# Kernel tuning notes

Measured on AMD Instinct MI355X. Metric: run time of the kernel, lower is better.

## Reference

```python
import jax, jax.numpy as jnp
import numpy as np

CHUNK = 128  # intra-chunk causal block size for the chunked linear-attention scan


def setup_inputs() -> dict:
    key = jax.random.key(0)
    ks = jax.random.split(key, 7)
    B, H, N, D, F = 1, 24, 4096, 128, 256
    q = jax.random.normal(ks[0], (B, H, N, D), dtype=jnp.float32)
    k = jax.random.normal(ks[1], (B, H, N, D), dtype=jnp.float32)
    v = jax.random.normal(ks[2], (B, H, N, D), dtype=jnp.float32)
    # fan-in scaling so phi features / accumulated state stay numerically sane
    w1 = jax.random.normal(ks[3], (F, D), dtype=jnp.float32) * (D ** -0.5)
    b1 = jax.random.normal(ks[4], (F,), dtype=jnp.float32) * 0.02
    w2 = jax.random.normal(ks[5], (F, F), dtype=jnp.float32) * (F ** -0.5)
    b2 = jax.random.normal(ks[6], (F,), dtype=jnp.float32) * 0.02
    return {"q": q, "k": k, "v": v, "w1": w1, "b1": b1, "w2": w2, "b2": b2}


def _phi(x, w1, b1, w2, b2):
    # Linear(D->F) -> SiLU -> Linear(F->F)
    h = jax.nn.silu(jnp.einsum('bnd,fd->bnf', x, w1) + b1)
    return jnp.einsum('bnf,gf->bng', h, w2) + b2


def _causal_scan(qp, kp, vf):
    # out_t = q_t . (sum_{s<=t} k_s v_s^T) / (t+1), chunked parallel form.
    BH, N, F = qp.shape
    D = vf.shape[-1]
    C = CHUNK
    nC = N // C
    qc = qp.reshape(BH, nC, C, F).transpose(1, 0, 2, 3)  # [nC,BH,C,F]
    kc = kp.reshape(BH, nC, C, F).transpose(1, 0, 2, 3)
    vc = vf.reshape(BH, nC, C, D).transpose(1, 0, 2, 3)
    offsets = (jnp.arange(nC) * C).astype(qp.dtype)
    mask = jnp.tril(jnp.ones((C, C), dtype=qp.dtype))  # include diagonal
    pos = jnp.arange(1, C + 1, dtype=qp.dtype)

    def step(w, inp):
        qb, kb, vb, off = inp
        inter = jnp.einsum('bcf,bfd->bcd', qb, w)
        attn = jnp.einsum('bcf,bsf->bcs', qb, kb) * mask
        intra = jnp.einsum('bcs,bsd->bcd', attn, vb)
        counts = off + pos  # global (token_idx + 1)
        out = (inter + intra) / counts[None, :, None]
        w = w + jnp.einsum('bcf,bcd->bfd', kb, vb)
        return w, out

    w0 = jnp.zeros((BH, F, D), dtype=qp.dtype)
    _, outs = jax.lax.scan(step, w0, (qc, kc, vc, offsets))  # outs [nC,BH,C,D]
    return outs.transpose(1, 0, 2, 3).reshape(BH, N, D)


def reference(q, k, v, w1, b1, w2, b2):
    B, H, N, D = q.shape
    qf = q.reshape(B * H, N, D)
    kf = k.reshape(B * H, N, D)
    vf = v.reshape(B * H, N, D)
    qp = _phi(qf, w1, b1, w2, b2)
    kp = _phi(kf, w1, b1, w2, b2)
    out_fwd = _causal_scan(qp, kp, vf)
    out_rev = _causal_scan(qp[:, ::-1], kp[:, ::-1], vf[:, ::-1])[:, ::-1]
    return (out_fwd + out_rev).reshape(B, H, N, D)
```

## Files before the change

kernel.cpp:

```cpp
#include <hip/hip_runtime.h>


typedef __attribute__((ext_vector_type(8))) _Float16 f16x8;
typedef __attribute__((ext_vector_type(4))) _Float16 f16x4;
typedef __attribute__((ext_vector_type(4))) float f32x4;

#define MFMA16(a, b, c) __builtin_amdgcn_mfma_f32_16x16x32_f16((a), (b), (c), 0, 0, 0)

constexpr int BH   = 24;
constexpr int NSEQ = 4096;
constexpr int DD   = 128;
constexpr int FF   = 256;
constexpr int CHK  = 128;
constexpr int NC   = NSEQ / CHK;
constexpr int NROWS = BH * NSEQ;

__global__ void prep_kernel(const float* __restrict__ w1, const float* __restrict__ w2,
                            _Float16* __restrict__ w1h, _Float16* __restrict__ w2h) {
  int i = blockIdx.x * 256 + threadIdx.x;
  if (i < FF * DD) w1h[i] = (_Float16)w1[i];
  if (i < FF * FF) w2h[i] = (_Float16)w2[i];
}

__global__ void vt_kernel(const float* __restrict__ v, _Float16* __restrict__ vT) {
  __shared__ __align__(16) _Float16 lt[128][136];
  int blk = blockIdx.x;
  int c = blk & 31, bh = blk >> 5;
  const float* vc = v + ((size_t)bh * NSEQ + c * CHK) * DD;
  int tid = threadIdx.x;
#pragma unroll
  for (int it = 0; it < 16; ++it) {
    int flat = it * 1024 + tid * 4;
    int s = flat >> 7, d0 = flat & 127;
    float4 xv = *(const float4*)&vc[(size_t)s * DD + d0];
    lt[d0 + 0][s] = (_Float16)xv.x;
    lt[d0 + 1][s] = (_Float16)xv.y;
    lt[d0 + 2][s] = (_Float16)xv.z;
    lt[d0 + 3][s] = (_Float16)xv.w;
  }
  __syncthreads();
#pragma unroll
  for (int it = 0; it < 8; ++it) {
    int flat = it * 256 + tid;
    int d = flat >> 4, sg = flat & 15;
    *(f16x8*)&vT[((size_t)bh * DD + d) * NSEQ + c * CHK + sg * 8] =
        *(const f16x8*)&lt[d][sg * 8];
  }
}

__global__ __launch_bounds__(512, 2)
void phi_kernel(const float* __restrict__ q, const float* __restrict__ k,
                const float* __restrict__ b1, const float* __restrict__ b2,
                const _Float16* __restrict__ w1h, const _Float16* __restrict__ w2h,
                _Float16* __restrict__ qp, _Float16* __restrict__ kp,
                _Float16* __restrict__ kpT) {
  __shared__ __align__(16) char smem[137216];
  _Float16 (*xs)[136]  = (_Float16(*)[136])smem;
  _Float16 (*w1s)[136] = (_Float16(*)[136])(smem + 34816);
  _Float16 (*hs)[264]  = (_Float16(*)[264])smem;
  _Float16 (*w2s)[136] = (_Float16(*)[136])(smem + 67584);
  int blk = blockIdx.x;
  const float* src;
  _Float16* dst;
  bool isk;
  int rb;
  if (blk < NROWS / 128) { src = q; dst = qp; rb = blk * 128; isk = false; }
  else                   { src = k; dst = kp; rb = (blk - NROWS / 128) * 128; isk = true; }
  int tid = threadIdx.x;
  int lane = tid & 63, wv = tid >> 6, lr = lane & 15, lq = lane >> 4;

#pragma unroll
  for (int it = 0; it < 8; ++it) {
    int flat = it * 512 + tid;
    int f = flat >> 4, cg = flat & 15;
    *(f16x8*)&w1s[f][cg * 8] = *(const f16x8*)&w1h[f * DD + cg * 8];
  }
#pragma unroll
  for (int it = 0; it < 8; ++it) {
    int flat = it * 512 + tid;
    int r = flat >> 5, dg = flat & 31;
    float4 xv = *(const float4*)&src[(size_t)(rb + r) * DD + dg * 4];
    f16x4 hv = {(_Float16)xv.x, (_Float16)xv.y, (_Float16)xv.z, (_Float16)xv.w};
    *(f16x4*)&xs[r][dg * 4] = hv;
  }
  __syncthreads();

  int wm1 = wv & 1, wn1 = wv >> 1;
  f32x4 acc[4][4] = {};
#pragma unroll
  for (int ks = 0; ks < 4; ++ks) {
    f16x8 av[4];
#pragma unroll
    for (int im = 0; im < 4; ++im)
      av[im] = *(const f16x8*)&xs[wm1 * 64 + im * 16 + lr][ks * 32 + lq * 8];
#pragma unroll
    for (int fn = 0; fn < 4; ++fn) {
      f16x8 bv = *(const f16x8*)&w1s[wn1 * 64 + fn * 16 + lr][ks * 32 + lq * 8];
#pragma unroll
      for (int im = 0; im < 4; ++im) acc[im][fn] = MFMA16(av[im], bv, acc[im][fn]);
    }
  }
  __syncthreads();

#pragma unroll
  for (int it = 0; it < 8; ++it) {
    int flat = it * 512 + tid;
    int g = flat >> 4, cg = flat & 15;
    *(f16x8*)&w2s[g][cg * 8] = *(const f16x8*)&w2h[(size_t)g * FF + cg * 8];
  }
#pragma unroll
  for (int im = 0; im < 4; ++im)
#pragma unroll
    for (int fn = 0; fn < 4; ++fn) {
      int f = wn1 * 64 + fn * 16 + lr;
      float bb = b1[f];
      int r0 = wm1 * 64 + im * 16 + lq * 4;
#pragma unroll
      for (int r = 0; r < 4; ++r) {
        float xv = acc[im][fn][r] + bb;
        hs[r0 + r][f] = (_Float16)(xv / (1.0f + __expf(-xv)));
      }
    }
  __syncthreads();

  int wmg = wv & 1, wng = wv >> 1;
  f32x4 ac2[4][4] = {};
#pragma unroll
  for (int ks = 0; ks < 4; ++ks) {
    f16x8 av[4];
#pragma unroll
    for (int im = 0; im < 4; ++im)
      av[im] = *(const f16x8*)&hs[wmg * 64 + im * 16 + lr][ks * 32 + lq * 8];
#pragma unroll
    for (int fn = 0; fn < 4; ++fn) {
      f16x8 bv = *(const f16x8*)&w2s[wng * 64 + fn * 16 + lr][ks * 32 + lq * 8];
#pragma unroll
      for (int im = 0; im < 4; ++im) ac2[im][fn] = MFMA16(av[im], bv, ac2[im][fn]);
    }
  }
  __syncthreads();
#pragma unroll
  for (int it = 0; it < 8; ++it) {
    int flat = it * 512 + tid;
    int g = flat >> 4, cg = flat & 15;
    *(f16x8*)&w2s[g][cg * 8] = *(const f16x8*)&w2h[(size_t)g * FF + 128 + cg * 8];
  }
  __syncthreads();
#pragma unroll
  for (int ks = 0; ks < 4; ++ks) {
    f16x8 av[4];
#pragma unroll
    for (int im = 0; im < 4; ++im)
      av[im] = *(const f16x8*)&hs[wmg * 64 + im * 16 + lr][128 + ks * 32 + lq * 8];
#pragma unroll
    for (int fn = 0; fn < 4; ++fn) {
      f16x8 bv = *(const f16x8*)&w2s[wng * 64 + fn * 16 + lr][ks * 32 + lq * 8];
#pragma unroll
      for (int im = 0; im < 4; ++im) ac2[im][fn] = MFMA16(av[im], bv, ac2[im][fn]);
    }
  }

  int bh = rb >> 12, s0 = rb & 4095;
#pragma unroll
  for (int im = 0; im < 4; ++im)
#pragma unroll
    for (int fn = 0; fn < 4; ++fn) {
      int g = wng * 64 + fn * 16 + lr;
      float bb = b2[g];
      int r0 = wmg * 64 + im * 16 + lq * 4;
#pragma unroll
      for (int r = 0; r < 4; ++r) {
        _Float16 val = (_Float16)(ac2[im][fn][r] + bb);
        dst[(size_t)(rb + r0 + r) * FF + g] = val;
        if (isk) kpT[((size_t)bh * FF + g) * NSEQ + s0 + r0 + r] = val;
      }
    }
}

__global__ __launch_bounds__(512, 2)
void s_kernel(const _Float16* __restrict__ vT, const _Float16* __restrict__ kpT,
              _Float16* __restrict__ S) {
  __shared__ __align__(16) _Float16 vt[128][136];
  __shared__ __align__(16) _Float16 kt[256][136];
  int blk = blockIdx.x;
  int c = blk & 31, bh = blk >> 5;
  int tid = threadIdx.x;
#pragma unroll
  for (int it = 0; it < 4; ++it) {
    int flat = it * 512 + tid;
    int d = flat >> 4, sg = flat & 15;
    *(f16x8*)&vt[d][sg * 8] = *(const f16x8*)&vT[((size_t)bh * DD + d) * NSEQ + c * CHK + sg * 8];
  }
#pragma unroll
  for (int it = 0; it < 8; ++it) {
    int flat = it * 512 + tid;
    int f = flat >> 4, sg = flat & 15;
    *(f16x8*)&kt[f][sg * 8] = *(const f16x8*)&kpT[((size_t)bh * FF + f) * NSEQ + c * CHK + sg * 8];
  }
  __syncthreads();
  int lane = tid & 63, wv = tid >> 6, lr = lane & 15, lq = lane >> 4;
  int wmd = wv & 1, wnf = wv >> 1;
  f32x4 acc[4][4] = {};
#pragma unroll
  for (int ks = 0; ks < 4; ++ks) {
    f16x8 av[4];
#pragma unroll
    for (int im = 0; im < 4; ++im)
      av[im] = *(const f16x8*)&vt[wmd * 64 + im * 16 + lr][ks * 32 + lq * 8];
#pragma unroll
    for (int fn = 0; fn < 4; ++fn) {
      f16x8 bv = *(const f16x8*)&kt[wnf * 64 + fn * 16 + lr][ks * 32 + lq * 8];
#pragma unroll
      for (int im = 0; im < 4; ++im) acc[im][fn] = MFMA16(av[im], bv, acc[im][fn]);
    }
  }
  _Float16* Sp = S + ((size_t)bh * NC + c) * (size_t)(DD * FF);
#pragma unroll
  for (int im = 0; im < 4; ++im)
#pragma unroll
    for (int fn = 0; fn < 4; ++fn) {
      int f = wnf * 64 + fn * 16 + lr;
#pragma unroll
      for (int r = 0; r < 4; ++r) {
        int d = wmd * 64 + im * 16 + lq * 4 + r;
        Sp[(size_t)d * FF + f] = (_Float16)acc[im][fn][r];
      }
    }
}

__global__ void prefix_kernel(_Float16* S_Wr, _Float16* __restrict__ Wf) {
  size_t idx = (size_t)blockIdx.x * 256 + threadIdx.x;
  int bh = (int)(idx >> 15);
  int df = (int)(idx & 32767);
  size_t base = (size_t)bh * NC * 32768 + df;
  float vals[NC];
#pragma unroll
  for (int c = 0; c < NC; ++c) vals[c] = (float)S_Wr[base + (size_t)c * 32768];
  float run = 0.f;
#pragma unroll
  for (int c = 0; c < NC; ++c) { Wf[base + (size_t)c * 32768] = (_Float16)run; run += vals[c]; }
  run = 0.f;
#pragma unroll
  for (int c = NC - 1; c >= 0; --c) { S_Wr[base + (size_t)c * 32768] = (_Float16)run; run += vals[c]; }
}

__global__ __launch_bounds__(512, 2)
void scan_kernel(const _Float16* __restrict__ qp, const _Float16* __restrict__ kp,
                 const _Float16* __restrict__ vT, const _Float16* __restrict__ Wf,
                 const _Float16* __restrict__ Wr, float* __restrict__ out) {
  __shared__ __align__(16) _Float16 vt[128][136];
  __shared__ __align__(16) _Float16 P[128][136];
  int blk = blockIdx.x;
  int c = blk & 31, bh = blk >> 5;
  const _Float16* qpc = qp + ((size_t)bh * NSEQ + c * CHK) * FF;
  const _Float16* kpc = kp + ((size_t)bh * NSEQ + c * CHK) * FF;
  int tid = threadIdx.x, lane = tid & 63, wv = tid >> 6, lr = lane & 15, lq = lane >> 4;
  int wm = wv & 3, wn = wv >> 2;

  f16x8 aq[2][8];
#pragma unroll
  for (int im = 0; im < 2; ++im)
#pragma unroll
    for (int ks = 0; ks < 8; ++ks)
      aq[im][ks] = *(const f16x8*)&qpc[(size_t)(wm * 32 + im * 16 + lr) * FF + ks * 32 + lq * 8];
#pragma unroll
  for (int it = 0; it < 4; ++it) {
    int flat = it * 512 + tid;
    int d = flat >> 4, sg = flat & 15;
    *(f16x8*)&vt[d][sg * 8] = *(const f16x8*)&vT[((size_t)bh * DD + d) * NSEQ + c * CHK + sg * 8];
  }
  f16x8 bk[2][8];
#pragma unroll
  for (int ks = 0; ks < 8; ++ks)
    bk[0][ks] = *(const f16x8*)&kpc[(size_t)(wn * 64 + lr) * FF + ks * 32 + lq * 8];
  f32x4 pacc[2][4] = {};
#pragma unroll
  for (int j = 0; j < 4; ++j) {
    int cur = j & 1;
    if (j < 3)
#pragma unroll
      for (int ks = 0; ks < 8; ++ks)
        bk[cur ^ 1][ks] = *(const f16x8*)&kpc[(size_t)(wn * 64 + (j + 1) * 16 + lr) * FF + ks * 32 + lq * 8];
#pragma unroll
    for (int ks = 0; ks < 8; ++ks)
#pragma unroll
      for (int im = 0; im < 2; ++im)
        pacc[im][j] = MFMA16(aq[im][ks], bk[cur][ks], pacc[im][j]);
  }
#pragma unroll
  for (int im = 0; im < 2; ++im)
#pragma unroll
    for (int j = 0; j < 4; ++j)
#pragma unroll
      for (int r = 0; r < 4; ++r)
        P[wm * 32 + im * 16 + lq * 4 + r][wn * 64 + j * 16 + lr] = (_Float16)pacc[im][j][r];

  const _Float16* Wfc = Wf + ((size_t)bh * NC + c) * (size_t)(DD * FF);
  const _Float16* Wrc = Wr + ((size_t)bh * NC + c) * (size_t)(DD * FF);
  f16x8 bf[8], br[8];
#pragma unroll
  for (int ks = 0; ks < 8; ++ks) {
    int d = wn * 64 + lr;
    bf[ks] = *(const f16x8*)&Wfc[(size_t)d * FF + ks * 32 + lq * 8];
    br[ks] = *(const f16x8*)&Wrc[(size_t)d * FF + ks * 32 + lq * 8];
  }
  __syncthreads();

  f32x4 af[2][4] = {}, ar[2][4] = {};
#pragma unroll
  for (int jd = 0; jd < 4; ++jd) {
#pragma unroll
    for (int ks = 0; ks < 8; ++ks)
#pragma unroll
      for (int im = 0; im < 2; ++im) {
        af[im][jd] = MFMA16(aq[im][ks], bf[ks], af[im][jd]);
        ar[im][jd] = MFMA16(aq[im][ks], br[ks], ar[im][jd]);
      }
    if (jd < 3)
#pragma unroll
      for (int ks = 0; ks < 8; ++ks) {
        int d = wn * 64 + (jd + 1) * 16 + lr;
        bf[ks] = *(const f16x8*)&Wfc[(size_t)d * FF + ks * 32 + lq * 8];
        br[ks] = *(const f16x8*)&Wrc[(size_t)d * FF + ks * 32 + lq * 8];
      }
    {
      int ks = jd;
      f16x8 bv[4];
#pragma unroll
      for (int jd2 = 0; jd2 < 4; ++jd2)
        bv[jd2] = *(const f16x8*)&vt[wn * 64 + jd2 * 16 + lr][ks * 32 + lq * 8];
#pragma unroll
      for (int im = 0; im < 2; ++im) {
        int irow = wm * 32 + im * 16 + lr;
        f16x8 p = *(const f16x8*)&P[irow][ks * 32 + lq * 8];
        f16x8 pf = p, pr = p;
#pragma unroll
        for (int jj = 0; jj < 8; ++jj) {
          int s = ks * 32 + lq * 8 + jj;
          pf[jj] = (s <= irow) ? p[jj] : (_Float16)0.0f;
          pr[jj] = (s >= irow) ? p[jj] : (_Float16)0.0f;
        }
#pragma unroll
        for (int jd2 = 0; jd2 < 4; ++jd2) {
          af[im][jd2] = MFMA16(pf, bv[jd2], af[im][jd2]);
          ar[im][jd2] = MFMA16(pr, bv[jd2], ar[im][jd2]);
        }
      }
    }
  }

  float* oc = out + ((size_t)bh * NSEQ + c * CHK) * DD;
#pragma unroll
  for (int im = 0; im < 2; ++im)
#pragma unroll
    for (int jd = 0; jd < 4; ++jd) {
      int d = wn * 64 + jd * 16 + lr;
#pragma unroll
      for (int r = 0; r < 4; ++r) {
        int il = wm * 32 + im * 16 + lq * 4 + r;
        int gi = c * CHK + il;
        oc[(size_t)il * DD + d] = af[im][jd][r] / (float)(gi + 1) + ar[im][jd][r] / (float)(NSEQ - gi);
      }
    }
}

extern "C" void kernel_launch(void* const* d_in, const int* in_sizes, int n_in,
                              void* d_out, int out_size, void* d_ws, size_t ws_size,
                              hipStream_t stream) {
  const float* q  = (const float*)d_in[0];
  const float* k  = (const float*)d_in[1];
  const float* v  = (const float*)d_in[2];
  const float* w1 = (const float*)d_in[3];
  const float* b1 = (const float*)d_in[4];
  const float* w2 = (const float*)d_in[5];
  const float* b2 = (const float*)d_in[6];
  float* out = (float*)d_out;

  char* ws = (char*)d_ws;
  const size_t SZ = 50331648ull;
  _Float16* w1h = (_Float16*)(ws);
  _Float16* w2h = (_Float16*)(ws + 65536);
  _Float16* qp  = (_Float16*)(ws + 196608);
  _Float16* kp  = (_Float16*)(ws + 196608 + SZ);
  _Float16* kpT = (_Float16*)(ws + 196608 + 2 * SZ);
  _Float16* S   = (_Float16*)(ws + 196608 + 3 * SZ);
  _Float16* vT  = (_Float16*)(ws + 196608 + 4 * SZ);
  _Float16* Wf  = kpT;
  _Float16* Wr  = S;

  prep_kernel<<<dim3(256), dim3(256), 0, stream>>>(w1, w2, w1h, w2h);
  vt_kernel<<<dim3(BH * NC), dim3(256), 0, stream>>>(v, vT);
  phi_kernel<<<dim3(2 * NROWS / 128), dim3(512), 0, stream>>>(q, k, b1, b2, w1h, w2h, qp, kp, kpT);
  s_kernel<<<dim3(BH * NC), dim3(512), 0, stream>>>(vT, kpT, S);
  prefix_kernel<<<dim3(BH * DD * FF / 256), dim3(256), 0, stream>>>(S, Wf);
  scan_kernel<<<dim3(BH * NC), dim3(512), 0, stream>>>(qp, kp, vT, Wf, Wr, out);
}
```

Baseline: 416.9 us.

## Stage phi outputs through LDS for coalesced stores and widen block to 1024 threads

phi_kernel now writes its fp16 outputs into shared memory, both row-major and transposed, and then issues 16-byte vector stores to qp/kp and kpT. Before, each thread wrote scattered 2-byte values, and the kpT stores used a large stride. The block grows to 16 waves with a 4x2 wave tiling, so each wave holds half as many accumulators. Both halves of w2 are prefetched into registers at kernel start, hiding their global latency behind the first GEMM. The cost is one more barrier, more LDS traffic and higher register pressure from the prefetch buffers.

Result: faster. 405.1 us (-2.8%).

```diff
diff --git a/kernel.cpp b/kernel.cpp
--- a/kernel.cpp
+++ b/kernel.cpp
@@ -48,7 +48,7 @@
   }
 }
 
-__global__ __launch_bounds__(512, 2)
+__global__ __launch_bounds__(1024, 4)
 void phi_kernel(const float* __restrict__ q, const float* __restrict__ k,
                 const float* __restrict__ b1, const float* __restrict__ b2,
                 const _Float16* __restrict__ w1h, const _Float16* __restrict__ w2h,
@@ -59,6 +59,8 @@
   _Float16 (*w1s)[136] = (_Float16(*)[136])(smem + 34816);
   _Float16 (*hs)[264]  = (_Float16(*)[264])smem;
   _Float16 (*w2s)[136] = (_Float16(*)[136])(smem + 67584);
+  _Float16 (*os)[264]  = (_Float16(*)[264])smem;
+  _Float16 (*ot)[136]  = (_Float16(*)[136])(smem + 67584);
   int blk = blockIdx.x;
   const float* src;
   _Float16* dst;
@@ -68,16 +70,25 @@
   else                   { src = k; dst = kp; rb = (blk - NROWS / 128) * 128; isk = true; }
   int tid = threadIdx.x;
   int lane = tid & 63, wv = tid >> 6, lr = lane & 15, lq = lane >> 4;
-
-#pragma unroll
-  for (int it = 0; it < 8; ++it) {
-    int flat = it * 512 + tid;
+  int wm = wv & 3, wn = wv >> 2;
+
+  f16x8 p0r[4], p1r[4];
+#pragma unroll
+  for (int it = 0; it < 4; ++it) {
+    int flat = it * 1024 + tid;
+    int g = flat >> 4, cg = flat & 15;
+    p0r[it] = *(const f16x8*)&w2h[(size_t)g * FF + cg * 8];
+    p1r[it] = *(const f16x8*)&w2h[(size_t)g * FF + 128 + cg * 8];
+  }
+#pragma unroll
+  for (int it = 0; it < 4; ++it) {
+    int flat = it * 1024 + tid;
     int f = flat >> 4, cg = flat & 15;
     *(f16x8*)&w1s[f][cg * 8] = *(const f16x8*)&w1h[f * DD + cg * 8];
   }
 #pragma unroll
-  for (int it = 0; it < 8; ++it) {
-    int flat = it * 512 + tid;
+  for (int it = 0; it < 4; ++it) {
+    int flat = it * 1024 + tid;
     int r = flat >> 5, dg = flat & 31;
     float4 xv = *(const float4*)&src[(size_t)(rb + r) * DD + dg * 4];
     f16x4 hv = {(_Float16)xv.x, (_Float16)xv.y, (_Float16)xv.z, (_Float16)xv.w};
@@ -85,36 +96,35 @@
   }
   __syncthreads();
 
-  int wm1 = wv & 1, wn1 = wv >> 1;
-  f32x4 acc[4][4] = {};
+  f32x4 acc[2][4] = {};
 #pragma unroll
   for (int ks = 0; ks < 4; ++ks) {
-    f16x8 av[4];
-#pragma unroll
-    for (int im = 0; im < 4; ++im)
-      av[im] = *(const f16x8*)&xs[wm1 * 64 + im * 16 + lr][ks * 32 + lq * 8];
-#pragma unroll
-    for (int fn = 0; fn < 4; ++fn) {
-      f16x8 bv = *(const f16x8*)&w1s[wn1 * 64 + fn * 16 + lr][ks * 32 + lq * 8];
-#pragma unroll
-      for (int im = 0; im < 4; ++im) acc[im][fn] = MFMA16(av[im], bv, acc[im][fn]);
-    }
-  }
-  __syncthreads();
-
-#pragma unroll
-  for (int it = 0; it < 8; ++it) {
-    int flat = it * 512 + tid;
+    f16x8 av[2];
+#pragma unroll
+    for (int im = 0; im < 2; ++im)
+      av[im] = *(const f16x8*)&xs[wm * 32 + im * 16 + lr][ks * 32 + lq * 8];
+#pragma unroll
+    for (int fn = 0; fn < 4; ++fn) {
+      f16x8 bv = *(const f16x8*)&w1s[wn * 64 + fn * 16 + lr][ks * 32 + lq * 8];
+#pragma unroll
+      for (int im = 0; im < 2; ++im) acc[im][fn] = MFMA16(av[im], bv, acc[im][fn]);
+    }
+  }
+  __syncthreads();
+
+#pragma unroll
+  for (int it = 0; it < 4; ++it) {
+    int flat = it * 1024 + tid;
     int g = flat >> 4, cg = flat & 15;
-    *(f16x8*)&w2s[g][cg * 8] = *(const f16x8*)&w2h[(size_t)g * FF + cg * 8];
-  }
-#pragma unroll
-  for (int im = 0; im < 4; ++im)
-#pragma unroll
-    for (int fn = 0; fn < 4; ++fn) {
-      int f = wn1 * 64 + fn * 16 + lr;
+    *(f16x8*)&w2s[g][cg * 8] = p0r[it];
+  }
+#pragma unroll
+  for (int im = 0; im < 2; ++im)
+#pragma unroll
+    for (int fn = 0; fn < 4; ++fn) {
+      int f = wn * 64 + fn * 16 + lr;
       float bb = b1[f];
-      int r0 = wm1 * 64 + im * 16 + lq * 4;
+      int r0 = wm * 32 + im * 16 + lq * 4;
 #pragma unroll
       for (int r = 0; r < 4; ++r) {
         float xv = acc[im][fn][r] + bb;
@@ -123,58 +133,73 @@
     }
   __syncthreads();
 
-  int wmg = wv & 1, wng = wv >> 1;
-  f32x4 ac2[4][4] = {};
+  f32x4 ac2[2][4] = {};
 #pragma unroll
   for (int ks = 0; ks < 4; ++ks) {
-    f16x8 av[4];
-#pragma unroll
-    for (int im = 0; im < 4; ++im)
-      av[im] = *(const f16x8*)&hs[wmg * 64 + im * 16 + lr][ks * 32 + lq * 8];
-#pragma unroll
-    for (int fn = 0; fn < 4; ++fn) {
-      f16x8 bv = *(const f16x8*)&w2s[wng * 64 + fn * 16 + lr][ks * 32 + lq * 8];
-#pragma unroll
-      for (int im = 0; im < 4; ++im) ac2[im][fn] = MFMA16(av[im], bv, ac2[im][fn]);
-    }
-  }
-  __syncthreads();
-#pragma unroll
-  for (int it = 0; it < 8; ++it) {
-    int flat = it * 512 + tid;
+    f16x8 av[2];
+#pragma unroll
+    for (int im = 0; im < 2; ++im)
+      av[im] = *(const f16x8*)&hs[wm * 32 + im * 16 + lr][ks * 32 + lq * 8];
+#pragma unroll
+    for (int fn = 0; fn < 4; ++fn) {
+      f16x8 bv = *(const f16x8*)&w2s[wn * 64 + fn * 16 + lr][ks * 32 + lq * 8];
+#pragma unroll
+      for (int im = 0; im < 2; ++im) ac2[im][fn] = MFMA16(av[im], bv, ac2[im][fn]);
+    }
+  }
+  __syncthreads();
+#pragma unroll
+  for (int it = 0; it < 4; ++it) {
+    int flat = it * 1024 + tid;
     int g = flat >> 4, cg = flat & 15;
-    *(f16x8*)&w2s[g][cg * 8] = *(const f16x8*)&w2h[(size_t)g * FF + 128 + cg * 8];
+    *(f16x8*)&w2s[g][cg * 8] = p1r[it];
   }
   __syncthreads();
 #pragma unroll
   for (int ks = 0; ks < 4; ++ks) {
-    f16x8 av[4];
-#pragma unroll
-    for (int im = 0; im < 4; ++im)
-      av[im] = *(const f16x8*)&hs[wmg * 64 + im * 16 + lr][128 + ks * 32 + lq * 8];
-#pragma unroll
-    for (int fn = 0; fn < 4; ++fn) {
-      f16x8 bv = *(const f16x8*)&w2s[wng * 64 + fn * 16 + lr][ks * 32 + lq * 8];
-#pragma unroll
-      for (int im = 0; im < 4; ++im) ac2[im][fn] = MFMA16(av[im], bv, ac2[im][fn]);
-    }
-  }
+    f16x8 av[2];
+#pragma unroll
+    for (int im = 0; im < 2; ++im)
+      av[im] = *(const f16x8*)&hs[wm * 32 + im * 16 + lr][128 + ks * 32 + lq * 8];
+#pragma unroll
+    for (int fn = 0; fn < 4; ++fn) {
+      f16x8 bv = *(const f16x8*)&w2s[wn * 64 + fn * 16 + lr][ks * 32 + lq * 8];
+#pragma unroll
+      for (int im = 0; im < 2; ++im) ac2[im][fn] = MFMA16(av[im], bv, ac2[im][fn]);
+    }
+  }
+  __syncthreads();
 
   int bh = rb >> 12, s0 = rb & 4095;
 #pragma unroll
-  for (int im = 0; im < 4; ++im)
-#pragma unroll
-    for (int fn = 0; fn < 4; ++fn) {
-      int g = wng * 64 + fn * 16 + lr;
+  for (int im = 0; im < 2; ++im)
+#pragma unroll
+    for (int fn = 0; fn < 4; ++fn) {
+      int g = wn * 64 + fn * 16 + lr;
       float bb = b2[g];
-      int r0 = wmg * 64 + im * 16 + lq * 4;
+      int r0 = wm * 32 + im * 16 + lq * 4;
 #pragma unroll
       for (int r = 0; r < 4; ++r) {
         _Float16 val = (_Float16)(ac2[im][fn][r] + bb);
-        dst[(size_t)(rb + r0 + r) * FF + g] = val;
-        if (isk) kpT[((size_t)bh * FF + g) * NSEQ + s0 + r0 + r] = val;
-      }
-    }
+        os[r0 + r][g] = val;
+        if (isk) ot[g][r0 + r] = val;
+      }
+    }
+  __syncthreads();
+#pragma unroll
+  for (int it = 0; it < 4; ++it) {
+    int flat = it * 1024 + tid;
+    int r = flat >> 5, cg = flat & 31;
+    *(f16x8*)&dst[(size_t)(rb + r) * FF + cg * 8] = *(const f16x8*)&os[r][cg * 8];
+  }
+  if (isk) {
+#pragma unroll
+    for (int it = 0; it < 4; ++it) {
+      int flat = it * 1024 + tid;
+      int f = flat >> 4, sg = flat & 15;
+      *(f16x8*)&kpT[((size_t)bh * FF + f) * NSEQ + s0 + sg * 8] = *(const f16x8*)&ot[f][sg * 8];
+    }
+  }
 }
 
 __global__ __launch_bounds__(512, 2)
@@ -390,7 +415,7 @@
 
   prep_kernel<<<dim3(256), dim3(256), 0, stream>>>(w1, w2, w1h, w2h);
   vt_kernel<<<dim3(BH * NC), dim3(256), 0, stream>>>(v, vT);
-  phi_kernel<<<dim3(2 * NROWS / 128), dim3(512), 0, stream>>>(q, k, b1, b2, w1h, w2h, qp, kp, kpT);
+  phi_kernel<<<dim3(2 * NROWS / 128), dim3(1024), 0, stream>>>(q, k, b1, b2, w1h, w2h, qp, kp, kpT);
   s_kernel<<<dim3(BH * NC), dim3(512), 0, stream>>>(vT, kpT, S);
   prefix_kernel<<<dim3(BH * DD * FF / 256), dim3(256), 0, stream>>>(S, Wf);
   scan_kernel<<<dim3(BH * NC), dim3(512), 0, stream>>>(qp, kp, vT, Wf, Wr, out);
```
